# Kernel optimization log

Hardware: AMD Instinct MI355X
Metric: run time of the kernel (lower is better)

Reference implementation:

```python
import jax, jax.numpy as jnp
import numpy as np

NEG = -1.0e9


def setup_inputs() -> dict:
    key = jax.random.key(0)
    ks = jax.random.split(key, 8)
    B, L, D = 4, 2048, 1024
    s = 1.0 / np.sqrt(D)
    return {
        "x": jax.random.normal(ks[0], (B, L, D), dtype=jnp.float32),
        "Wq": jax.random.normal(ks[1], (D, D), dtype=jnp.float32) * s,
        "bq": jax.random.normal(ks[2], (D,), dtype=jnp.float32) * 0.02,
        "Wk": jax.random.normal(ks[3], (D, D), dtype=jnp.float32) * s,
        "bk": jax.random.normal(ks[4], (D,), dtype=jnp.float32) * 0.02,
        "Wv": jax.random.normal(ks[5], (D, D), dtype=jnp.float32) * s,
        "bv": jax.random.normal(ks[6], (D,), dtype=jnp.float32) * 0.02,
        "lengths": jax.random.randint(ks[7], (B,), 1, 2048, dtype=jnp.int32),
    }


def reference(x, Wq, bq, Wk, bk, Wv, bv, lengths):
    # x: [B, L, D]; single-head self-attention with causal + length additive masks
    B, L, D = x.shape
    q = x @ Wq + bq  # [B, L, D]
    k = x @ Wk + bk
    v = x @ Wv + bv
    scale = 1.0 / jnp.sqrt(jnp.asarray(D, dtype=x.dtype))
    att = jnp.einsum("bid,bjd->bij", q, k) * scale  # [B, L, L]
    idx = jnp.arange(L)
    causal = jnp.where(idx[None, :] > idx[:, None], NEG, 0.0).astype(x.dtype)  # [L, L]
    # length mask: NEG where j >= len[b] or i >= len[b]
    invalid = (idx[None, :] >= lengths[:, None])  # [B, L]
    lenmask = jnp.where(invalid[:, :, None] | invalid[:, None, :], NEG, 0.0).astype(x.dtype)
    att = att + causal[None, :, :] + lenmask
    att = jax.nn.softmax(att, axis=-1)
    return jnp.einsum("bij,bjd->bid", att, v)
```

## Files before the change

kernel.cpp:

```cpp
#include <hip/hip_runtime.h>

#define NEGV (-1.0e9f)

typedef __bf16 bf16_t;
typedef __bf16 bf16x8 __attribute__((ext_vector_type(8)));
typedef __bf16 bf16x4 __attribute__((ext_vector_type(4)));
typedef float  f32x4  __attribute__((ext_vector_type(4)));

__device__ __forceinline__ void gld16(const void* g, void* l) {
    __builtin_amdgcn_global_load_lds(
        (const __attribute__((address_space(1))) void*)g,
        (__attribute__((address_space(3))) void*)l, 16, 0, 0);
}

__device__ __forceinline__ void nt_mainloop_db(
    const bf16_t* __restrict__ A, const bf16_t* __restrict__ B,
    int ldA, int ldB, int numKsteps,
    bf16_t* Atile, bf16_t* Btile,
    int tid, f32x4 acc[4][4])
{
    const int w    = tid >> 6;
    const int lane = tid & 63;
    const int wm   = w & 1;
    const int wn   = w >> 1;
    const int srow = lane >> 2;
    const int skc  = ((lane & 3) ^ ((lane >> 3) & 3)) * 8;
    const int quad = lane >> 4;
    const int l16  = lane & 15;
    const int sw   = (l16 >> 1) & 3;

    const bf16_t* ga0 = A + (size_t)((w * 2 + 0) * 16 + srow) * ldA + skc;
    const bf16_t* ga1 = A + (size_t)((w * 2 + 1) * 16 + srow) * ldA + skc;
    const bf16_t* gb0 = B + (size_t)((w * 2 + 0) * 16 + srow) * ldB + skc;
    const bf16_t* gb1 = B + (size_t)((w * 2 + 1) * 16 + srow) * ldB + skc;
    const int la0 = (w * 2 + 0) * 16 * 32;
    const int la1 = (w * 2 + 1) * 16 * 32;

    gld16(ga0, Atile + la0);
    gld16(ga1, Atile + la1);
    gld16(gb0, Btile + la0);
    gld16(gb1, Btile + la1);
    ga0 += 32; ga1 += 32; gb0 += 32; gb1 += 32;

    for (int kt = 0; kt < numKsteps; ++kt) {
        const int cur = (kt & 1) * (128 * 32);
        const int nxt = ((kt + 1) & 1) * (128 * 32);
        __syncthreads();
        if (kt + 1 < numKsteps) {
            gld16(ga0, Atile + nxt + la0);
            gld16(ga1, Atile + nxt + la1);
            gld16(gb0, Btile + nxt + la0);
            gld16(gb1, Btile + nxt + la1);
            ga0 += 32; ga1 += 32; gb0 += 32; gb1 += 32;
        }
        bf16x8 af[4], bfr[4];
#pragma unroll
        for (int i = 0; i < 4; ++i)
            af[i] = *(const bf16x8*)&Atile[cur + (wm * 64 + i * 16 + l16) * 32 + ((quad ^ sw) * 8)];
#pragma unroll
        for (int j = 0; j < 4; ++j)
            bfr[j] = *(const bf16x8*)&Btile[cur + (wn * 64 + j * 16 + l16) * 32 + ((quad ^ sw) * 8)];
#pragma unroll
        for (int i = 0; i < 4; ++i)
#pragma unroll
            for (int j = 0; j < 4; ++j)
                acc[i][j] = __builtin_amdgcn_mfma_f32_16x16x32_bf16(af[i], bfr[j], acc[i][j], 0, 0, 0);
    }
}

__global__ __launch_bounds__(256)
void convert_x_kernel(const float* __restrict__ x, bf16_t* __restrict__ xb)
{
    const size_t i = ((size_t)blockIdx.x * 256 + threadIdx.x) * 8;
    float4 a = *(const float4*)&x[i];
    float4 b = *(const float4*)&x[i + 4];
    bf16x8 o;
    o[0] = (bf16_t)a.x; o[1] = (bf16_t)a.y; o[2] = (bf16_t)a.z; o[3] = (bf16_t)a.w;
    o[4] = (bf16_t)b.x; o[5] = (bf16_t)b.y; o[6] = (bf16_t)b.z; o[7] = (bf16_t)b.w;
    *(bf16x8*)&xb[i] = o;
}

__global__ __launch_bounds__(256)
void transpose_w_kernel(const float* __restrict__ W0, const float* __restrict__ W1,
                        const float* __restrict__ W2, bf16_t* __restrict__ WT)
{
    __shared__ float t[32][33];
    const float* W = (blockIdx.z == 0) ? W0 : (blockIdx.z == 1) ? W1 : W2;
    bf16_t* WTz = WT + (size_t)blockIdx.z * 1024 * 1024;
    const int k0 = blockIdx.y * 32, n0 = blockIdx.x * 32;
    const int r = threadIdx.x >> 3, c4 = (threadIdx.x & 7) * 4;
    float4 v = *(const float4*)&W[(size_t)(k0 + r) * 1024 + n0 + c4];
    t[r][c4 + 0] = v.x; t[r][c4 + 1] = v.y; t[r][c4 + 2] = v.z; t[r][c4 + 3] = v.w;
    __syncthreads();
    bf16x4 o;
#pragma unroll
    for (int j = 0; j < 4; ++j) o[j] = (bf16_t)t[c4 + j][r];
    *(bf16x4*)&WTz[(size_t)(n0 + r) * 1024 + k0 + c4] = o;
}

__global__ __launch_bounds__(256)
void gemm_qk_kernel(const bf16_t* __restrict__ A, const bf16_t* __restrict__ Bt,
                    const float* __restrict__ bq, const float* __restrict__ bk,
                    bf16_t* __restrict__ C, int N, int Kd)
{
    __shared__ bf16_t Atile[2 * 128 * 32];
    __shared__ bf16_t Btile[2 * 128 * 32];
    const int tid = threadIdx.x;
    const int m0 = blockIdx.y * 128, n0 = blockIdx.x * 128;

    f32x4 acc[4][4];
#pragma unroll
    for (int i = 0; i < 4; ++i)
#pragma unroll
        for (int j = 0; j < 4; ++j) acc[i][j] = (f32x4)(0.0f);

    nt_mainloop_db(A + (size_t)m0 * Kd, Bt + (size_t)n0 * Kd, Kd, Kd, Kd / 32,
                   Atile, Btile, tid, acc);

    const int w = tid >> 6, lane = tid & 63;
    const int wm = w & 1, wn = w >> 1, quad = lane >> 4, l16 = lane & 15;
#pragma unroll
    for (int j = 0; j < 4; ++j) {
        const int col = n0 + wn * 64 + j * 16 + l16;
        const float bval = (col < 1024) ? bq[col] : bk[col - 1024];
#pragma unroll
        for (int i = 0; i < 4; ++i) {
#pragma unroll
            for (int r = 0; r < 4; ++r) {
                const int row = m0 + wm * 64 + i * 16 + quad * 4 + r;
                C[(size_t)row * N + col] = (bf16_t)(acc[i][j][r] + bval);
            }
        }
    }
}

__global__ __launch_bounds__(256)
void gemm_vt_kernel(const bf16_t* __restrict__ WvT, const bf16_t* __restrict__ xb,
                    const float* __restrict__ bv, bf16_t* __restrict__ VT,
                    int N, int Kd)
{
    __shared__ bf16_t Atile[2 * 128 * 32];
    __shared__ bf16_t Btile[2 * 128 * 32];
    const int tid = threadIdx.x;
    const int m0 = blockIdx.y * 128, n0 = blockIdx.x * 128;

    f32x4 acc[4][4];
#pragma unroll
    for (int i = 0; i < 4; ++i)
#pragma unroll
        for (int j = 0; j < 4; ++j) acc[i][j] = (f32x4)(0.0f);

    nt_mainloop_db(WvT + (size_t)m0 * Kd, xb + (size_t)n0 * Kd, Kd, Kd, Kd / 32,
                   Atile, Btile, tid, acc);

    const int w = tid >> 6, lane = tid & 63;
    const int wm = w & 1, wn = w >> 1, quad = lane >> 4, l16 = lane & 15;
#pragma unroll
    for (int i = 0; i < 4; ++i) {
#pragma unroll
        for (int r = 0; r < 4; ++r) {
            const int row = m0 + wm * 64 + i * 16 + quad * 4 + r;
            const float bval = bv[row];
#pragma unroll
            for (int j = 0; j < 4; ++j) {
                const int col = n0 + wn * 64 + j * 16 + l16;
                VT[(size_t)row * N + col] = (bf16_t)(acc[i][j][r] + bval);
            }
        }
    }
}

__global__ __launch_bounds__(256)
void scores_mfma_kernel(const bf16_t* __restrict__ Q, const bf16_t* __restrict__ K,
                        int ldq, const int* __restrict__ lengths,
                        float* __restrict__ S, int L, int Dd, float alpha)
{
    const int b = blockIdx.z;
    const int len = lengths[b];
    int it = (int)((sqrtf(8.0f * blockIdx.x + 1.0f) - 1.0f) * 0.5f);
    while ((it + 1) * (it + 2) / 2 <= (int)blockIdx.x) ++it;
    while (it * (it + 1) / 2 > (int)blockIdx.x) --it;
    const int jt = blockIdx.x - it * (it + 1) / 2;
    const int m0 = it * 128, n0 = jt * 128;
    float* Sb = S + (size_t)b * L * L;
    const int tid = threadIdx.x;

    __shared__ bf16_t Atile[2 * 128 * 32];
    __shared__ bf16_t Btile[2 * 128 * 32];
    f32x4 acc[4][4];
#pragma unroll
    for (int i = 0; i < 4; ++i)
#pragma unroll
        for (int j = 0; j < 4; ++j) acc[i][j] = (f32x4)(0.0f);

    const bf16_t* Qb = Q + (size_t)b * L * ldq + (size_t)m0 * ldq;
    const bf16_t* Kb = K + (size_t)b * L * ldq + (size_t)n0 * ldq;
    nt_mainloop_db(Qb, Kb, ldq, ldq, Dd / 32, Atile, Btile, tid, acc);

    const int w = tid >> 6, lane = tid & 63;
    const int wm = w & 1, wn = w >> 1, quad = lane >> 4, l16 = lane & 15;
#pragma unroll
    for (int i = 0; i < 4; ++i) {
#pragma unroll
        for (int j = 0; j < 4; ++j) {
            const int col = n0 + wn * 64 + j * 16 + l16;
#pragma unroll
            for (int r = 0; r < 4; ++r) {
                const int row = m0 + wm * 64 + i * 16 + quad * 4 + r;
                float s = acc[i][j][r] * alpha;
                if (col > row) s += NEGV;
                if (row >= len || col >= len) s += NEGV;
                Sb[(size_t)row * L + col] = s;
            }
        }
    }
}

__global__ __launch_bounds__(256)
void softmax_kernel(const float* __restrict__ S, bf16_t* __restrict__ P,
                    int L, int ldp)
{
    __shared__ float red[8];
    const int i = blockIdx.x;
    const int bound = ((i >> 7) + 1) << 7;
    const float* row = S + ((size_t)blockIdx.y * L + i) * L;
    bf16_t* prow = P + ((size_t)blockIdx.y * L + i) * ldp;
    const int t = threadIdx.x;
    const int w = t >> 6, lane = t & 63;
    const int j8 = t * 8;
    const bool act = j8 < bound;

    float v[8];
    float m = -3.0e38f;
    if (act) {
        float4 a = *(const float4*)&row[j8];
        float4 b = *(const float4*)&row[j8 + 4];
        v[0] = a.x; v[1] = a.y; v[2] = a.z; v[3] = a.w;
        v[4] = b.x; v[5] = b.y; v[6] = b.z; v[7] = b.w;
#pragma unroll
        for (int j = 0; j < 8; ++j) m = fmaxf(m, v[j]);
    }
#pragma unroll
    for (int off = 32; off > 0; off >>= 1) m = fmaxf(m, __shfl_down(m, off, 64));
    if (lane == 0) red[w] = m;
    __syncthreads();
    m = fmaxf(fmaxf(red[0], red[1]), fmaxf(red[2], red[3]));

    float s = 0.f;
    if (act) {
#pragma unroll
        for (int j = 0; j < 8; ++j) {
            v[j] = __expf(v[j] - m);
            s += v[j];
        }
    }
#pragma unroll
    for (int off = 32; off > 0; off >>= 1) s += __shfl_down(s, off, 64);
    if (lane == 0) red[4 + w] = s;
    __syncthreads();
    s = red[4] + red[5] + red[6] + red[7];

    if (act) {
        const float inv = 1.0f / s;
        bf16x8 o;
#pragma unroll
        for (int j = 0; j < 8; ++j) o[j] = (bf16_t)(v[j] * inv);
        *(bf16x8*)&prow[j8] = o;
    }
}

__global__ __launch_bounds__(256)
void pv_mfma_kernel(const bf16_t* __restrict__ P, int ldp,
                    const bf16_t* __restrict__ VT, int ldv,
                    float* __restrict__ O, int L, int Dd)
{
    __shared__ bf16_t Atile[2 * 128 * 32];
    __shared__ bf16_t Btile[2 * 128 * 32];
    const int b = blockIdx.z;
    const int mt = gridDim.y - 1 - blockIdx.y;
    const int m0 = mt * 128, n0 = blockIdx.x * 128;
    const int tid = threadIdx.x;

    f32x4 acc[4][4];
#pragma unroll
    for (int i = 0; i < 4; ++i)
#pragma unroll
        for (int j = 0; j < 4; ++j) acc[i][j] = (f32x4)(0.0f);

    const int ksteps = (m0 + 128) / 32;
    const bf16_t* Pb = P + (size_t)b * L * ldp + (size_t)m0 * ldp;
    const bf16_t* Vb = VT + (size_t)b * L + (size_t)n0 * ldv;
    nt_mainloop_db(Pb, Vb, ldp, ldv, ksteps, Atile, Btile, tid, acc);

    float* Ob = O + (size_t)b * L * Dd;
    const int w = tid >> 6, lane = tid & 63;
    const int wm = w & 1, wn = w >> 1, quad = lane >> 4, l16 = lane & 15;
#pragma unroll
    for (int i = 0; i < 4; ++i) {
#pragma unroll
        for (int j = 0; j < 4; ++j) {
            const int col = n0 + wn * 64 + j * 16 + l16;
#pragma unroll
            for (int r = 0; r < 4; ++r) {
                const int row = m0 + wm * 64 + i * 16 + quad * 4 + r;
                Ob[(size_t)row * Dd + col] = acc[i][j][r];
            }
        }
    }
}

extern "C" void kernel_launch(void* const* d_in, const int* in_sizes, int n_in,
                              void* d_out, int out_size, void* d_ws, size_t ws_size,
                              hipStream_t stream)
{
    const float* x  = (const float*)d_in[0];
    const float* Wq = (const float*)d_in[1];
    const float* bq = (const float*)d_in[2];
    const float* Wk = (const float*)d_in[3];
    const float* bk = (const float*)d_in[4];
    const float* Wv = (const float*)d_in[5];
    const float* bv = (const float*)d_in[6];
    const int*  len = (const int*)d_in[7];
    float* out = (float*)d_out;

    const int B = 4, L = 2048, D = 1024;
    const int M = B * L;
    const int N2 = 2 * D;

    bf16_t* xb = (bf16_t*)d_ws;
    bf16_t* WT = xb + (size_t)M * D;
    bf16_t* QK = WT + (size_t)3 * D * D;
    bf16_t* VT = QK + (size_t)M * N2;
    float*  S  = (float*)(VT + (size_t)D * M);
    bf16_t* P  = QK;

    convert_x_kernel<<<(M * D) / 2048, 256, 0, stream>>>(x, xb);

    transpose_w_kernel<<<dim3(32, 32, 3), 256, 0, stream>>>(Wq, Wk, Wv, WT);

    gemm_qk_kernel<<<dim3(N2 / 128, M / 128), 256, 0, stream>>>(
        xb, WT, bq, bk, QK, N2, D);

    gemm_vt_kernel<<<dim3(M / 128, D / 128), 256, 0, stream>>>(
        WT + (size_t)2 * D * D, xb, bv, VT, M, D);

    scores_mfma_kernel<<<dim3(136, 1, B), 256, 0, stream>>>(
        QK, QK + 1024, N2, len, S, L, D, 0.03125f);

    softmax_kernel<<<dim3(L, B), 256, 0, stream>>>(S, P, L, N2);

    pv_mfma_kernel<<<dim3(D / 128, L / 128, B), 256, 0, stream>>>(
        P, N2, VT, M, out, L, D);
}
```

Before: 272.4 us.

## Move all GEMMs to a 256x256 tiled, 512-thread, phase-pipelined MFMA mainloop

Replaces the 128x128 double-buffered NT mainloop with a 256x256 tile mainloop run by 8 waves. It uses an XOR-swizzled LDS layout and four staged phases per 64-wide K step that interleave async global-to-LDS loads with MFMA bursts under raised wave priority. The QK, V, scores and PV kernels move to the larger tiles, and the QK GEMM gets a block-index swizzle for L2 locality. Softmax now zero-fills P out to the 256-aligned causal bound so PV can read whole 256-wide K tiles. Each block uses 128KB of LDS and holds more accumulators, so occupancy drops and the causal kernels waste more work on diagonal tiles.

```diff
diff --git a/kernel.cpp b/kernel.cpp
--- a/kernel.cpp
+++ b/kernel.cpp
@@ -13,58 +13,90 @@
         (__attribute__((address_space(3))) void*)l, 16, 0, 0);
 }
 
-__device__ __forceinline__ void nt_mainloop_db(
+
+#define STG(P0, P1, BASE, NB, HOFS) do {               \
+    gld16(P0, (BASE) + (NB) * 32768 + (HOFS));         \
+    gld16(P1, (BASE) + (NB) * 32768 + (HOFS) + 8192);  \
+    P0 += 64; P1 += 64; } while (0)
+
+#define MMROW(ai)                                                                                    \
+    acc[ib + ai][0] = __builtin_amdgcn_mfma_f32_16x16x32_bf16(a##ai, b0, acc[ib + ai][0], 0, 0, 0);  \
+    acc[ib + ai][1] = __builtin_amdgcn_mfma_f32_16x16x32_bf16(a##ai, b1, acc[ib + ai][1], 0, 0, 0);  \
+    acc[ib + ai][2] = __builtin_amdgcn_mfma_f32_16x16x32_bf16(a##ai, b2, acc[ib + ai][2], 0, 0, 0);  \
+    acc[ib + ai][3] = __builtin_amdgcn_mfma_f32_16x16x32_bf16(a##ai, b3, acc[ib + ai][3], 0, 0, 0)
+
+#define PHASE(BUFO, HOFS, PK, STAGE_STMT, ENDW) do {                     \
+    bf16x8 a0 = *(const bf16x8*)(rdA + (BUFO) + (HOFS)        + (PK));   \
+    bf16x8 a1 = *(const bf16x8*)(rdA + (BUFO) + (HOFS) + 2048 + (PK));   \
+    bf16x8 a2 = *(const bf16x8*)(rdA + (BUFO) + (HOFS) + 4096 + (PK));   \
+    bf16x8 a3 = *(const bf16x8*)(rdA + (BUFO) + (HOFS) + 6144 + (PK));   \
+    bf16x8 b0 = *(const bf16x8*)(rdB + (BUFO)          + (PK));          \
+    bf16x8 b1 = *(const bf16x8*)(rdB + (BUFO) + 2048   + (PK));          \
+    bf16x8 b2 = *(const bf16x8*)(rdB + (BUFO) + 4096   + (PK));          \
+    bf16x8 b3 = *(const bf16x8*)(rdB + (BUFO) + 6144   + (PK));          \
+    STAGE_STMT;                                                          \
+    __builtin_amdgcn_s_barrier();                                        \
+    asm volatile("s_waitcnt lgkmcnt(0)" ::: "memory");                   \
+    __builtin_amdgcn_s_setprio(1);                                       \
+    {                                                                    \
+        const int ib = (HOFS) ? 4 : 0;                                   \
+        MMROW(0); MMROW(1); MMROW(2); MMROW(3);                          \
+    }                                                                    \
+    __builtin_amdgcn_s_setprio(0);                                       \
+    ENDW;                                                                \
+    __builtin_amdgcn_s_barrier();                                        \
+} while (0)
+
+__device__ __forceinline__ void mainloop256(
     const bf16_t* __restrict__ A, const bf16_t* __restrict__ B,
-    int ldA, int ldB, int numKsteps,
-    bf16_t* Atile, bf16_t* Btile,
-    int tid, f32x4 acc[4][4])
+    int ldA, int ldB, int nkt, char* smem, int tid, f32x4 acc[8][4])
 {
     const int w    = tid >> 6;
     const int lane = tid & 63;
     const int wm   = w & 1;
     const int wn   = w >> 1;
-    const int srow = lane >> 2;
-    const int skc  = ((lane & 3) ^ ((lane >> 3) & 3)) * 8;
+    const int l16  = lane & 15;
     const int quad = lane >> 4;
-    const int l16  = lane & 15;
-    const int sw   = (l16 >> 1) & 3;
-
-    const bf16_t* ga0 = A + (size_t)((w * 2 + 0) * 16 + srow) * ldA + skc;
-    const bf16_t* ga1 = A + (size_t)((w * 2 + 1) * 16 + srow) * ldA + skc;
-    const bf16_t* gb0 = B + (size_t)((w * 2 + 0) * 16 + srow) * ldB + skc;
-    const bf16_t* gb1 = B + (size_t)((w * 2 + 1) * 16 + srow) * ldB + skc;
-    const int la0 = (w * 2 + 0) * 16 * 32;
-    const int la1 = (w * 2 + 1) * 16 * 32;
-
-    gld16(ga0, Atile + la0);
-    gld16(ga1, Atile + la1);
-    gld16(gb0, Btile + la0);
-    gld16(gb1, Btile + la1);
-    ga0 += 32; ga1 += 32; gb0 += 32; gb1 += 32;
-
-    for (int kt = 0; kt < numKsteps; ++kt) {
-        const int cur = (kt & 1) * (128 * 32);
-        const int nxt = ((kt + 1) & 1) * (128 * 32);
-        __syncthreads();
-        if (kt + 1 < numKsteps) {
-            gld16(ga0, Atile + nxt + la0);
-            gld16(ga1, Atile + nxt + la1);
-            gld16(gb0, Btile + nxt + la0);
-            gld16(gb1, Btile + nxt + la1);
-            ga0 += 32; ga1 += 32; gb0 += 32; gb1 += 32;
-        }
-        bf16x8 af[4], bfr[4];
-#pragma unroll
-        for (int i = 0; i < 4; ++i)
-            af[i] = *(const bf16x8*)&Atile[cur + (wm * 64 + i * 16 + l16) * 32 + ((quad ^ sw) * 8)];
-#pragma unroll
-        for (int j = 0; j < 4; ++j)
-            bfr[j] = *(const bf16x8*)&Btile[cur + (wn * 64 + j * 16 + l16) * 32 + ((quad ^ sw) * 8)];
-#pragma unroll
-        for (int i = 0; i < 4; ++i)
-#pragma unroll
-            for (int j = 0; j < 4; ++j)
-                acc[i][j] = __builtin_amdgcn_mfma_f32_16x16x32_bf16(af[i], bfr[j], acc[i][j], 0, 0, 0);
+
+    const int r0 = tid >> 3;
+    const int c0 = ((tid & 7) ^ (r0 & 7)) * 8;
+    const int s1 = 512 + tid;
+    const int r1 = s1 >> 3;
+    const int c1 = ((s1 & 7) ^ (r1 & 7)) * 8;
+
+    const bf16_t* pa00 = A + (size_t)(r0)       * ldA + c0;
+    const bf16_t* pa01 = A + (size_t)(r1)       * ldA + c1;
+    const bf16_t* pa10 = A + (size_t)(128 + r0) * ldA + c0;
+    const bf16_t* pa11 = A + (size_t)(128 + r1) * ldA + c1;
+    const bf16_t* pb00 = B + (size_t)(r0)       * ldB + c0;
+    const bf16_t* pb01 = B + (size_t)(r1)       * ldB + c1;
+    const bf16_t* pb10 = B + (size_t)(128 + r0) * ldB + c0;
+    const bf16_t* pb11 = B + (size_t)(128 + r1) * ldB + c1;
+
+    char* const stA = smem + (w << 10);
+    char* const stB = smem + 65536 + (w << 10);
+
+    const int pk0 = ((quad    ) ^ (l16 & 7)) << 4;
+    const int pk1 = ((quad + 4) ^ (l16 & 7)) << 4;
+    const char* rdA = smem +         ((wm << 7) + l16) * 128;
+    const char* rdB = smem + 65536 + ((wn << 6) + l16) * 128;
+
+    STG(pa00, pa01, stA, 0, 0);
+    STG(pa10, pa11, stA, 0, 16384);
+    STG(pb00, pb01, stB, 0, 0);
+    STG(pb10, pb11, stB, 0, 16384);
+    asm volatile("s_waitcnt vmcnt(0)" ::: "memory");
+    __builtin_amdgcn_s_barrier();
+
+    for (int kt = 0; kt < nkt; ++kt) {
+        const int bufo = (kt & 1) << 15;
+        const int nb   = (kt & 1) ^ 1;
+        const bool st  = (kt + 1) < nkt;
+        PHASE(bufo, 0,    pk0, if (st) STG(pa00, pa01, stA, nb, 0),     );
+        PHASE(bufo, 0,    pk1, if (st) STG(pa10, pa11, stA, nb, 16384), );
+        PHASE(bufo, 8192, pk0, if (st) STG(pb00, pb01, stB, nb, 0),     );
+        PHASE(bufo, 8192, pk1, if (st) STG(pb10, pb11, stB, nb, 16384),
+              asm volatile("s_waitcnt vmcnt(0)" ::: "memory"));
     }
 }
 
@@ -98,24 +130,26 @@
     *(bf16x4*)&WTz[(size_t)(n0 + r) * 1024 + k0 + c4] = o;
 }
 
-__global__ __launch_bounds__(256)
-void gemm_qk_kernel(const bf16_t* __restrict__ A, const bf16_t* __restrict__ Bt,
-                    const float* __restrict__ bq, const float* __restrict__ bk,
-                    bf16_t* __restrict__ C, int N, int Kd)
-{
-    __shared__ bf16_t Atile[2 * 128 * 32];
-    __shared__ bf16_t Btile[2 * 128 * 32];
+__global__ __launch_bounds__(512, 2)
+void gemm_qk256(const bf16_t* __restrict__ A, const bf16_t* __restrict__ Bt,
+                const float* __restrict__ bq, const float* __restrict__ bk,
+                bf16_t* __restrict__ C, int N, int Kd)
+{
+    __shared__ __align__(16) char smem[131072];
+    int bid = blockIdx.y * 8 + blockIdx.x;
+    bid = (bid & 7) * 32 + (bid >> 3);
+    const int n0 = (bid & 7) * 256;
+    const int m0 = (bid >> 3) * 256;
     const int tid = threadIdx.x;
-    const int m0 = blockIdx.y * 128, n0 = blockIdx.x * 128;
-
-    f32x4 acc[4][4];
-#pragma unroll
-    for (int i = 0; i < 4; ++i)
+
+    f32x4 acc[8][4];
+#pragma unroll
+    for (int i = 0; i < 8; ++i)
 #pragma unroll
         for (int j = 0; j < 4; ++j) acc[i][j] = (f32x4)(0.0f);
 
-    nt_mainloop_db(A + (size_t)m0 * Kd, Bt + (size_t)n0 * Kd, Kd, Kd, Kd / 32,
-                   Atile, Btile, tid, acc);
+    mainloop256(A + (size_t)m0 * Kd, Bt + (size_t)n0 * Kd, Kd, Kd, Kd >> 6,
+                smem, tid, acc);
 
     const int w = tid >> 6, lane = tid & 63;
     const int wm = w & 1, wn = w >> 1, quad = lane >> 4, l16 = lane & 15;
@@ -124,89 +158,85 @@
         const int col = n0 + wn * 64 + j * 16 + l16;
         const float bval = (col < 1024) ? bq[col] : bk[col - 1024];
 #pragma unroll
-        for (int i = 0; i < 4; ++i) {
-#pragma unroll
-            for (int r = 0; r < 4; ++r) {
-                const int row = m0 + wm * 64 + i * 16 + quad * 4 + r;
-                C[(size_t)row * N + col] = (bf16_t)(acc[i][j][r] + bval);
-            }
-        }
-    }
-}
-
-__global__ __launch_bounds__(256)
-void gemm_vt_kernel(const bf16_t* __restrict__ WvT, const bf16_t* __restrict__ xb,
-                    const float* __restrict__ bv, bf16_t* __restrict__ VT,
-                    int N, int Kd)
-{
-    __shared__ bf16_t Atile[2 * 128 * 32];
-    __shared__ bf16_t Btile[2 * 128 * 32];
+        for (int i = 0; i < 8; ++i) {
+            const int row = m0 + wm * 128 + i * 16 + quad * 4;
+#pragma unroll
+            for (int r = 0; r < 4; ++r)
+                C[(size_t)(row + r) * N + col] = (bf16_t)(acc[i][j][r] + bval);
+        }
+    }
+}
+
+__global__ __launch_bounds__(512, 2)
+void gemm_vt256(const bf16_t* __restrict__ WvT, const bf16_t* __restrict__ xb,
+                const float* __restrict__ bv, bf16_t* __restrict__ VT,
+                int N, int Kd)
+{
+    __shared__ __align__(16) char smem[131072];
+    const int m0 = blockIdx.y * 256, n0 = blockIdx.x * 256;
     const int tid = threadIdx.x;
-    const int m0 = blockIdx.y * 128, n0 = blockIdx.x * 128;
-
-    f32x4 acc[4][4];
-#pragma unroll
-    for (int i = 0; i < 4; ++i)
+
+    f32x4 acc[8][4];
+#pragma unroll
+    for (int i = 0; i < 8; ++i)
 #pragma unroll
         for (int j = 0; j < 4; ++j) acc[i][j] = (f32x4)(0.0f);
 
-    nt_mainloop_db(WvT + (size_t)m0 * Kd, xb + (size_t)n0 * Kd, Kd, Kd, Kd / 32,
-                   Atile, Btile, tid, acc);
+    mainloop256(WvT + (size_t)m0 * Kd, xb + (size_t)n0 * Kd, Kd, Kd, Kd >> 6,
+                smem, tid, acc);
 
     const int w = tid >> 6, lane = tid & 63;
     const int wm = w & 1, wn = w >> 1, quad = lane >> 4, l16 = lane & 15;
 #pragma unroll
-    for (int i = 0; i < 4; ++i) {
+    for (int i = 0; i < 8; ++i) {
+        const int row = m0 + wm * 128 + i * 16 + quad * 4;
 #pragma unroll
         for (int r = 0; r < 4; ++r) {
-            const int row = m0 + wm * 64 + i * 16 + quad * 4 + r;
-            const float bval = bv[row];
+            const float bval = bv[row + r];
 #pragma unroll
             for (int j = 0; j < 4; ++j) {
                 const int col = n0 + wn * 64 + j * 16 + l16;
-                VT[(size_t)row * N + col] = (bf16_t)(acc[i][j][r] + bval);
+                VT[(size_t)(row + r) * N + col] = (bf16_t)(acc[i][j][r] + bval);
             }
         }
     }
 }
 
-__global__ __launch_bounds__(256)
-void scores_mfma_kernel(const bf16_t* __restrict__ Q, const bf16_t* __restrict__ K,
-                        int ldq, const int* __restrict__ lengths,
-                        float* __restrict__ S, int L, int Dd, float alpha)
-{
+__global__ __launch_bounds__(512, 2)
+void scores256(const bf16_t* __restrict__ Q, const bf16_t* __restrict__ K,
+               int ldq, const int* __restrict__ lengths,
+               float* __restrict__ S, int L, int Dd, float alpha)
+{
+    __shared__ __align__(16) char smem[131072];
     const int b = blockIdx.z;
     const int len = lengths[b];
-    int it = (int)((sqrtf(8.0f * blockIdx.x + 1.0f) - 1.0f) * 0.5f);
+    int it = 0;
     while ((it + 1) * (it + 2) / 2 <= (int)blockIdx.x) ++it;
-    while (it * (it + 1) / 2 > (int)blockIdx.x) --it;
     const int jt = blockIdx.x - it * (it + 1) / 2;
-    const int m0 = it * 128, n0 = jt * 128;
+    const int m0 = it * 256, n0 = jt * 256;
     float* Sb = S + (size_t)b * L * L;
     const int tid = threadIdx.x;
 
-    __shared__ bf16_t Atile[2 * 128 * 32];
-    __shared__ bf16_t Btile[2 * 128 * 32];
-    f32x4 acc[4][4];
-#pragma unroll
-    for (int i = 0; i < 4; ++i)
+    f32x4 acc[8][4];
+#pragma unroll
+    for (int i = 0; i < 8; ++i)
 #pragma unroll
         for (int j = 0; j < 4; ++j) acc[i][j] = (f32x4)(0.0f);
 
     const bf16_t* Qb = Q + (size_t)b * L * ldq + (size_t)m0 * ldq;
     const bf16_t* Kb = K + (size_t)b * L * ldq + (size_t)n0 * ldq;
-    nt_mainloop_db(Qb, Kb, ldq, ldq, Dd / 32, Atile, Btile, tid, acc);
+    mainloop256(Qb, Kb, ldq, ldq, Dd >> 6, smem, tid, acc);
 
     const int w = tid >> 6, lane = tid & 63;
     const int wm = w & 1, wn = w >> 1, quad = lane >> 4, l16 = lane & 15;
 #pragma unroll
-    for (int i = 0; i < 4; ++i) {
+    for (int i = 0; i < 8; ++i) {
 #pragma unroll
         for (int j = 0; j < 4; ++j) {
             const int col = n0 + wn * 64 + j * 16 + l16;
 #pragma unroll
             for (int r = 0; r < 4; ++r) {
-                const int row = m0 + wm * 64 + i * 16 + quad * 4 + r;
+                const int row = m0 + wm * 128 + i * 16 + quad * 4 + r;
                 float s = acc[i][j][r] * alpha;
                 if (col > row) s += NEGV;
                 if (row >= len || col >= len) s += NEGV;
@@ -222,7 +252,8 @@
 {
     __shared__ float red[8];
     const int i = blockIdx.x;
-    const int bound = ((i >> 7) + 1) << 7;
+    const int bound  = ((i >> 7) + 1) << 7;
+    const int bound2 = ((i >> 8) + 1) << 8;
     const float* row = S + ((size_t)blockIdx.y * L + i) * L;
     bf16_t* prow = P + ((size_t)blockIdx.y * L + i) * ldp;
     const int t = threadIdx.x;
@@ -266,45 +297,48 @@
 #pragma unroll
         for (int j = 0; j < 8; ++j) o[j] = (bf16_t)(v[j] * inv);
         *(bf16x8*)&prow[j8] = o;
-    }
-}
-
-__global__ __launch_bounds__(256)
-void pv_mfma_kernel(const bf16_t* __restrict__ P, int ldp,
-                    const bf16_t* __restrict__ VT, int ldv,
-                    float* __restrict__ O, int L, int Dd)
-{
-    __shared__ bf16_t Atile[2 * 128 * 32];
-    __shared__ bf16_t Btile[2 * 128 * 32];
+    } else if (j8 < bound2) {
+        bf16x8 z;
+#pragma unroll
+        for (int j = 0; j < 8; ++j) z[j] = (bf16_t)0.0f;
+        *(bf16x8*)&prow[j8] = z;
+    }
+}
+
+__global__ __launch_bounds__(512, 2)
+void pv256(const bf16_t* __restrict__ P, int ldp,
+           const bf16_t* __restrict__ VT, int ldv,
+           float* __restrict__ O, int L, int Dd)
+{
+    __shared__ __align__(16) char smem[131072];
     const int b = blockIdx.z;
     const int mt = gridDim.y - 1 - blockIdx.y;
-    const int m0 = mt * 128, n0 = blockIdx.x * 128;
+    const int m0 = mt * 256, n0 = blockIdx.x * 256;
     const int tid = threadIdx.x;
 
-    f32x4 acc[4][4];
-#pragma unroll
-    for (int i = 0; i < 4; ++i)
+    f32x4 acc[8][4];
+#pragma unroll
+    for (int i = 0; i < 8; ++i)
 #pragma unroll
         for (int j = 0; j < 4; ++j) acc[i][j] = (f32x4)(0.0f);
 
-    const int ksteps = (m0 + 128) / 32;
+    const int nkt = (m0 + 256) >> 6;
     const bf16_t* Pb = P + (size_t)b * L * ldp + (size_t)m0 * ldp;
     const bf16_t* Vb = VT + (size_t)b * L + (size_t)n0 * ldv;
-    nt_mainloop_db(Pb, Vb, ldp, ldv, ksteps, Atile, Btile, tid, acc);
+    mainloop256(Pb, Vb, ldp, ldv, nkt, smem, tid, acc);
 
     float* Ob = O + (size_t)b * L * Dd;
     const int w = tid >> 6, lane = tid & 63;
     const int wm = w & 1, wn = w >> 1, quad = lane >> 4, l16 = lane & 15;
 #pragma unroll
-    for (int i = 0; i < 4; ++i) {
+    for (int i = 0; i < 8; ++i) {
+        const int row = m0 + wm * 128 + i * 16 + quad * 4;
 #pragma unroll
         for (int j = 0; j < 4; ++j) {
             const int col = n0 + wn * 64 + j * 16 + l16;
 #pragma unroll
-            for (int r = 0; r < 4; ++r) {
-                const int row = m0 + wm * 64 + i * 16 + quad * 4 + r;
-                Ob[(size_t)row * Dd + col] = acc[i][j][r];
-            }
+            for (int r = 0; r < 4; ++r)
+                Ob[(size_t)(row + r) * Dd + col] = acc[i][j][r];
         }
     }
 }
@@ -338,17 +372,15 @@
 
     transpose_w_kernel<<<dim3(32, 32, 3), 256, 0, stream>>>(Wq, Wk, Wv, WT);
 
-    gemm_qk_kernel<<<dim3(N2 / 128, M / 128), 256, 0, stream>>>(
-        xb, WT, bq, bk, QK, N2, D);
-
-    gemm_vt_kernel<<<dim3(M / 128, D / 128), 256, 0, stream>>>(
+    gemm_qk256<<<dim3(8, 32), 512, 0, stream>>>(xb, WT, bq, bk, QK, N2, D);
+
+    gemm_vt256<<<dim3(32, 4), 512, 0, stream>>>(
         WT + (size_t)2 * D * D, xb, bv, VT, M, D);
 
-    scores_mfma_kernel<<<dim3(136, 1, B), 256, 0, stream>>>(
+    scores256<<<dim3(36, 1, B), 512, 0, stream>>>(
         QK, QK + 1024, N2, len, S, L, D, 0.03125f);
 
     softmax_kernel<<<dim3(L, B), 256, 0, stream>>>(S, P, L, N2);
 
-    pv_mfma_kernel<<<dim3(D / 128, L / 128, B), 256, 0, stream>>>(
-        P, N2, VT, M, out, L, D);
-}
+    pv256<<<dim3(4, 8, 4), 512, 0, stream>>>(P, N2, VT, M, out, L, D);
+}
```

Measured after the change: 280.7 us. 1.03x slower.
